# Kernel optimization log

Hardware: AMD Instinct MI355X
Metric: run time of the kernel (lower is better)

## Reference

```python
import jax, jax.numpy as jnp
import numpy as np

B, T, C, H = 2, 2048, 1024, 16
D = C // H  # head_dim = 64
CH = C // 2


def _ln(x, g, b, eps=1e-5):
    m = x.mean(-1, keepdims=True)
    v = ((x - m) ** 2).mean(-1, keepdims=True)
    return (x - m) / jnp.sqrt(v + eps) * g + b


def setup_inputs() -> dict:
    key = jax.random.key(0)
    ks = iter(jax.random.split(key, 32))
    w = lambda shp: jax.random.normal(next(ks), shp, dtype=jnp.float32) * 0.02
    inp = {
        'x': jax.random.normal(next(ks), (B, T, C), dtype=jnp.float32),
        'attention_mask': jnp.ones((B, T, T), dtype=jnp.int32),
        # importance_net: Linear(C,C/2), LN(C/2), GELU, Linear(C/2,1), Sigmoid
        'imp_w1': w((C, CH)), 'imp_b1': jnp.zeros((CH,)),
        'imp_g': jnp.ones((CH,)), 'imp_beta': jnp.zeros((CH,)),
        'imp_w2': w((CH, 1)), 'imp_b2': jnp.zeros((1,)),
        # reasoning_net: Linear(C,C), LN(C), GELU, Linear(C,C)
        'rsn_w1': w((C, C)), 'rsn_b1': jnp.zeros((C,)),
        'rsn_g': jnp.ones((C,)), 'rsn_beta': jnp.zeros((C,)),
        'rsn_w2': w((C, C)), 'rsn_b2': jnp.zeros((C,)),
        # attention projections
        'q_w': w((C, C)), 'q_b': jnp.zeros((C,)),
        'k_w': w((C, C)), 'k_b': jnp.zeros((C,)),
        'v_w': w((C, C)), 'v_b': jnp.zeros((C,)),
        'o_w': w((C, C)), 'o_b': jnp.zeros((C,)),
        # temp_net: Linear(C,C/2), LN(C/2), GELU, Linear(C/2,H)
        'tmp_w1': w((C, CH)), 'tmp_b1': jnp.zeros((CH,)),
        'tmp_g': jnp.ones((CH,)), 'tmp_beta': jnp.zeros((CH,)),
        'tmp_w2': w((CH, H)), 'tmp_b2': jnp.zeros((H,)),
        # output LayerNorm
        'norm_g': jnp.ones((C,)), 'norm_b': jnp.zeros((C,)),
    }
    return inp


def reference(x, attention_mask, imp_w1, imp_b1, imp_g, imp_beta, imp_w2, imp_b2,
              rsn_w1, rsn_b1, rsn_g, rsn_beta, rsn_w2, rsn_b2,
              q_w, q_b, k_w, k_b, v_w, v_b, o_w, o_b,
              tmp_w1, tmp_b1, tmp_g, tmp_beta, tmp_w2, tmp_b2,
              norm_g, norm_b):
    Bz, Tz, Cz = x.shape
    # importance gating: [B,T,1]
    h = jax.nn.gelu(_ln(x @ imp_w1 + imp_b1, imp_g, imp_beta), approximate=False)
    importance = jnp.maximum(jax.nn.sigmoid(h @ imp_w2 + imp_b2), 1e-6)
    xi = x * importance
    # reasoning net on gated input
    h = jax.nn.gelu(_ln(xi @ rsn_w1 + rsn_b1, rsn_g, rsn_beta), approximate=False)
    reasoned = h @ rsn_w2 + rsn_b2
    # projections
    q = (reasoned @ q_w + q_b).reshape(Bz, Tz, H, D).transpose(0, 2, 1, 3)
    k = (xi @ k_w + k_b).reshape(Bz, Tz, H, D).transpose(0, 2, 1, 3)
    v = (x @ v_w + v_b).reshape(Bz, Tz, H, D).transpose(0, 2, 1, 3)
    # per-(batch,head) temperature
    ht = jax.nn.gelu(_ln(reasoned.mean(axis=1) @ tmp_w1 + tmp_b1, tmp_g, tmp_beta), approximate=False)
    temp = jax.nn.softplus(ht @ tmp_w2 + tmp_b2) + 0.5  # [B,H]
    # attention with mask and learned temperature before softmax
    scale = 1.0 / jnp.sqrt(jnp.float32(D))
    attn = jnp.einsum('bhqd,bhkd->bhqk', q, k) * scale
    attn = jnp.where(attention_mask[:, None] == 0, -jnp.inf, attn)
    attn = attn * temp[:, :, None, None]
    attn = jax.nn.softmax(attn, axis=-1)
    # dropout is identity in eval mode
    out = jnp.einsum('bhqk,bhkd->bhqd', attn, v)
    out = out.transpose(0, 2, 1, 3).reshape(Bz, Tz, Cz)
    out = out @ o_w + o_b
    return _ln(x + out, norm_g, norm_b)
```

## Files before the change

kernel.cpp:

```cpp
#include <hip/hip_runtime.h>
#include <hip/hip_bf16.h>
#include <math.h>

#define BB 2
#define TT 2048
#define CC 1024
#define HH 16
#define DD 64
#define CHALF 512
#define NN (BB * TT)
#define LOG2E 1.44269504088896340736f

typedef __attribute__((ext_vector_type(8))) short short8;
typedef __attribute__((ext_vector_type(4))) short short4_t;
typedef __attribute__((ext_vector_type(4))) float f32x4;

__device__ __forceinline__ float gelu_exact(float x) {
    return 0.5f * x * (1.0f + erff(x * 0.70710678118654752f));
}

__device__ __forceinline__ short f2bf(float f) {
    __hip_bfloat16 h = __float2bfloat16(f);
    short s;
    __builtin_memcpy(&s, &h, 2);
    return s;
}

__device__ __forceinline__ short4_t pack_bf16x4(float a, float b, float c,
                                                float d) {
    short4_t s4;
    s4[0] = f2bf(a);
    s4[1] = f2bf(b);
    s4[2] = f2bf(c);
    s4[3] = f2bf(d);
    return s4;
}

__device__ __forceinline__ void async_copy16(const void* g, void* l) {
    __builtin_amdgcn_global_load_lds(
        (const __attribute__((address_space(1))) void*)g,
        (__attribute__((address_space(3))) void*)l, 16, 0, 0);
}

__global__ __launch_bounds__(256) void prep(
    const float* __restrict__ x, __hip_bfloat16* __restrict__ x_bf,
    const int* __restrict__ mask, int* __restrict__ flags,
    const float* w0, const float* w1, const float* w2, const float* w3,
    const float* w4, const float* w5, const float* w6,
    __hip_bfloat16* t0, __hip_bfloat16* t1, __hip_bfloat16* t2,
    __hip_bfloat16* t3, __hip_bfloat16* t4, __hip_bfloat16* t5,
    __hip_bfloat16* t6) {
    __shared__ float T[64][65];
    int blk = blockIdx.x;
    int tid = threadIdx.x;
    if (blk < 2048) {
        int i = (blk * 256 + tid) * 8;
        float4 a = *(const float4*)&x[i];
        float4 b = *(const float4*)&x[i + 4];
        __hip_bfloat16 o[8] = {
            __float2bfloat16(a.x), __float2bfloat16(a.y),
            __float2bfloat16(a.z), __float2bfloat16(a.w),
            __float2bfloat16(b.x), __float2bfloat16(b.y),
            __float2bfloat16(b.z), __float2bfloat16(b.w)};
        *(float4*)&x_bf[i] = *(float4*)o;
    } else if (blk < 4096) {
        int idx = blk - 2048;
        int kt = idx & 31, qt = (idx >> 5) & 31, b = idx >> 10;
        int* red = (int*)T;
        int r = tid >> 2;
        int c0 = (tid & 3) * 16;
        const int* base =
            mask + ((size_t)(b * TT + qt * 64 + r)) * TT + kt * 64 + c0;
        int all = 1;
#pragma unroll
        for (int i = 0; i < 4; ++i) {
            int4 m4 = *(const int4*)(base + i * 4);
            all &= (m4.x != 0) & (m4.y != 0) & (m4.z != 0) & (m4.w != 0);
        }
        red[tid] = all;
        __syncthreads();
#pragma unroll
        for (int o = 128; o > 0; o >>= 1) {
            if (tid < o) red[tid] &= red[tid + o];
            __syncthreads();
        }
        if (tid == 0) flags[(b * 32 + qt) * 32 + kt] = red[0];
    } else {
        int idx = blk - 4096;
        const float* W;
        __hip_bfloat16* Wt;
        int N, n0, k0;
        if (idx < 128) {
            W = w0; Wt = t0; N = 512;
            n0 = (idx & 7) * 64;
            k0 = (idx >> 3) * 64;
        } else {
            idx -= 128;
            int w = idx >> 8;
            int r = idx & 255;
            N = 1024;
            n0 = (r & 15) * 64;
            k0 = (r >> 4) * 64;
            switch (w) {
                case 0: W = w1; Wt = t1; break;
                case 1: W = w2; Wt = t2; break;
                case 2: W = w3; Wt = t3; break;
                case 3: W = w4; Wt = t4; break;
                case 4: W = w5; Wt = t5; break;
                default: W = w6; Wt = t6; break;
            }
        }
        int c = tid & 63, r4 = tid >> 6;
#pragma unroll
        for (int i = 0; i < 16; ++i) {
            int row = i * 4 + r4;
            T[row][c] = W[(size_t)(k0 + row) * N + n0 + c];
        }
        __syncthreads();
#pragma unroll
        for (int i = 0; i < 16; ++i) {
            int row = i * 4 + r4;
            Wt[(size_t)(n0 + row) * CC + k0 + c] = __float2bfloat16(T[c][row]);
        }
    }
}

template <bool BF16OUT>
__global__ __launch_bounds__(256) void gemm_mfma64(
    const short* __restrict__ A, const short* __restrict__ Wt,
    const float* __restrict__ bias, float* __restrict__ Cf,
    __hip_bfloat16* __restrict__ Cb, int M, int N, int K) {
    __shared__ short As0[64][32], As1[64][32];
    __shared__ short Bs0[128][32], Bs1[128][32];
    int tid = threadIdx.x;
    int wave = tid >> 6, lane = tid & 63;
    int m16 = lane & 15, quad = lane >> 4;
    int wm = wave >> 1, wn = wave & 1;
    int row0 = blockIdx.y * 64, col0 = blockIdx.x * 128;
    int lr = lane >> 2;
    int kof = (lane & 3) * 8;

    f32x4 acc[2][4];
#pragma unroll
    for (int i = 0; i < 2; ++i)
#pragma unroll
        for (int j = 0; j < 4; ++j) acc[i][j] = (f32x4){0.f, 0.f, 0.f, 0.f};

    for (int k0 = 0; k0 < K; k0 += 64) {
        const short* arow = A + (size_t)(row0 + wave * 16 + lr) * K + k0 + kof;
        async_copy16(arow, &As0[wave * 16][0]);
        async_copy16(arow + 32, &As1[wave * 16][0]);
#pragma unroll
        for (int j = 0; j < 2; ++j) {
            int rbase = wave * 32 + j * 16;
            const short* brow =
                Wt + (size_t)(col0 + rbase + lr) * K + k0 + kof;
            async_copy16(brow, &Bs0[rbase][0]);
            async_copy16(brow + 32, &Bs1[rbase][0]);
        }
        __syncthreads();
#pragma unroll
        for (int kc = 0; kc < 2; ++kc) {
            short8 af[2], bfr[4];
#pragma unroll
            for (int i = 0; i < 2; ++i)
                af[i] = kc ? *(const short8*)&As1[wm * 32 + i * 16 + m16][quad * 8]
                           : *(const short8*)&As0[wm * 32 + i * 16 + m16][quad * 8];
#pragma unroll
            for (int j = 0; j < 4; ++j)
                bfr[j] = kc ? *(const short8*)&Bs1[wn * 64 + j * 16 + m16][quad * 8]
                            : *(const short8*)&Bs0[wn * 64 + j * 16 + m16][quad * 8];
#pragma unroll
            for (int i = 0; i < 2; ++i)
#pragma unroll
                for (int j = 0; j < 4; ++j)
                    acc[i][j] = __builtin_amdgcn_mfma_f32_16x16x32_bf16(
                        af[i], bfr[j], acc[i][j], 0, 0, 0);
        }
        __syncthreads();
    }
#pragma unroll
    for (int i = 0; i < 2; ++i) {
#pragma unroll
        for (int j = 0; j < 4; ++j) {
            int col = col0 + wn * 64 + j * 16 + m16;
            float bv = bias[col];
#pragma unroll
            for (int rr = 0; rr < 4; ++rr) {
                int row = row0 + wm * 32 + i * 16 + quad * 4 + rr;
                float val = acc[i][j][rr] + bv;
                if (BF16OUT)
                    Cb[(size_t)row * N + col] = __float2bfloat16(val);
                else
                    Cf[(size_t)row * N + col] = val;
            }
        }
    }
}

__global__ __launch_bounds__(256) void gemm_qkv(
    const short* __restrict__ Aq, const short* __restrict__ Ak,
    const short* __restrict__ Av, const short* __restrict__ Wq,
    const short* __restrict__ Wk, const short* __restrict__ Wv,
    const float* __restrict__ bq, const float* __restrict__ bk,
    const float* __restrict__ bv, __hip_bfloat16* __restrict__ Cq,
    __hip_bfloat16* __restrict__ Ck, __hip_bfloat16* __restrict__ Cv,
    const float* __restrict__ tmp) {
    int z = blockIdx.z;
    const short* A = (z == 0) ? Aq : (z == 1) ? Ak : Av;
    const short* Wt = (z == 0) ? Wq : (z == 1) ? Wk : Wv;
    const float* bias = (z == 0) ? bq : (z == 1) ? bk : bv;

    __shared__ short As[128][32];
    __shared__ short Bs[128][32];
    int tid = threadIdx.x;
    int wave = tid >> 6, lane = tid & 63;
    int m16 = lane & 15, quad = lane >> 4;
    int wm = wave >> 1, wn = wave & 1;
    int row0 = blockIdx.y * 128, col0 = blockIdx.x * 128;
    int lr = lane >> 2;
    int kof = (lane & 3) * 8;

    float scale = 1.0f;
    if (z == 0)
        scale = tmp[(row0 >> 11) * HH + (col0 >> 6) + wn] * 0.125f * LOG2E;

    f32x4 acc[4][4];
#pragma unroll
    for (int i = 0; i < 4; ++i)
#pragma unroll
        for (int j = 0; j < 4; ++j) acc[i][j] = (f32x4){0.f, 0.f, 0.f, 0.f};

    for (int k0 = 0; k0 < CC; k0 += 32) {
#pragma unroll
        for (int j = 0; j < 2; ++j) {
            int rbase = wave * 32 + j * 16;
            async_copy16(A + (size_t)(row0 + rbase + lr) * CC + k0 + kof,
                         &As[rbase][0]);
            async_copy16(Wt + (size_t)(col0 + rbase + lr) * CC + k0 + kof,
                         &Bs[rbase][0]);
        }
        __syncthreads();
        short8 af[4], bfr[4];
#pragma unroll
        for (int i = 0; i < 4; ++i)
            af[i] = *(const short8*)&As[wm * 64 + i * 16 + m16][quad * 8];
#pragma unroll
        for (int j = 0; j < 4; ++j)
            bfr[j] = *(const short8*)&Bs[wn * 64 + j * 16 + m16][quad * 8];
#pragma unroll
        for (int i = 0; i < 4; ++i)
#pragma unroll
            for (int j = 0; j < 4; ++j)
                acc[i][j] = __builtin_amdgcn_mfma_f32_16x16x32_bf16(
                    af[i], bfr[j], acc[i][j], 0, 0, 0);
        __syncthreads();
    }
    if (z == 2) {
        int b = row0 >> 11;
        int t0r = (row0 & (TT - 1)) + wm * 64 + quad * 4;
#pragma unroll
        for (int i = 0; i < 4; ++i) {
#pragma unroll
            for (int j = 0; j < 4; ++j) {
                int col = col0 + wn * 64 + j * 16 + m16;
                int h = col >> 6, d = col & 63;
                float bv2 = bias[col];
                short4_t pk = pack_bf16x4(
                    acc[i][j][0] + bv2, acc[i][j][1] + bv2,
                    acc[i][j][2] + bv2, acc[i][j][3] + bv2);
                *(short4_t*)&Cv[(((size_t)(b * HH + h) * DD) + d) * TT + t0r +
                                i * 16] = pk;
            }
        }
    } else {
        __hip_bfloat16* C = (z == 0) ? Cq : Ck;
#pragma unroll
        for (int i = 0; i < 4; ++i) {
#pragma unroll
            for (int j = 0; j < 4; ++j) {
                int col = col0 + wn * 64 + j * 16 + m16;
                float bv2 = bias[col];
#pragma unroll
                for (int rr = 0; rr < 4; ++rr) {
                    int row = row0 + wm * 64 + i * 16 + quad * 4 + rr;
                    C[(size_t)row * CC + col] =
                        __float2bfloat16((acc[i][j][rr] + bv2) * scale);
                }
            }
        }
    }
}

__global__ __launch_bounds__(256) void imp_fused(
    const float* __restrict__ h1, const float* __restrict__ g,
    const float* __restrict__ beta, const float* __restrict__ w2,
    const float* __restrict__ b2, const float* __restrict__ x,
    __hip_bfloat16* __restrict__ xi) {
    int row = blockIdx.x;
    int tid = threadIdx.x;
    const float* hr = h1 + (size_t)row * CHALF;
    float v0 = hr[tid], v1 = hr[tid + 256];
    __shared__ float red[256];
    red[tid] = v0 + v1;
    __syncthreads();
#pragma unroll
    for (int o = 128; o > 0; o >>= 1) {
        if (tid < o) red[tid] += red[tid + o];
        __syncthreads();
    }
    float mean = red[0] * (1.0f / CHALF);
    __syncthreads();
    float d0 = v0 - mean, d1 = v1 - mean;
    red[tid] = d0 * d0 + d1 * d1;
    __syncthreads();
#pragma unroll
    for (int o = 128; o > 0; o >>= 1) {
        if (tid < o) red[tid] += red[tid + o];
        __syncthreads();
    }
    float inv = rsqrtf(red[0] * (1.0f / CHALF) + 1e-5f);
    __syncthreads();
    float ge0 = gelu_exact(d0 * inv * g[tid] + beta[tid]);
    float ge1 = gelu_exact(d1 * inv * g[tid + 256] + beta[tid + 256]);
    red[tid] = ge0 * w2[tid] + ge1 * w2[tid + 256];
    __syncthreads();
#pragma unroll
    for (int o = 128; o > 0; o >>= 1) {
        if (tid < o) red[tid] += red[tid + o];
        __syncthreads();
    }
    float z = red[0] + b2[0];
    float sg = 1.0f / (1.0f + expf(-z));
    float imp = fmaxf(sg, 1e-6f);
#pragma unroll
    for (int i = 0; i < 4; ++i) {
        int c = i * 256 + tid;
        xi[(size_t)row * CC + c] =
            __float2bfloat16(x[(size_t)row * CC + c] * imp);
    }
}

template <int WIDTH>
__global__ __launch_bounds__(256) void ln_gelu_bf16(
    const float* __restrict__ Y, const float* __restrict__ g,
    const float* __restrict__ beta, __hip_bfloat16* __restrict__ O) {
    constexpr int PT = WIDTH / 256;
    int row = blockIdx.x;
    int tid = threadIdx.x;
    const float* yr = Y + (size_t)row * WIDTH;
    float v[PT];
    float s = 0.f;
#pragma unroll
    for (int i = 0; i < PT; ++i) {
        v[i] = yr[i * 256 + tid];
        s += v[i];
    }
    __shared__ float red[256];
    red[tid] = s;
    __syncthreads();
#pragma unroll
    for (int o = 128; o > 0; o >>= 1) {
        if (tid < o) red[tid] += red[tid + o];
        __syncthreads();
    }
    float mean = red[0] * (1.0f / WIDTH);
    __syncthreads();
    s = 0.f;
#pragma unroll
    for (int i = 0; i < PT; ++i) {
        float d = v[i] - mean;
        s += d * d;
    }
    red[tid] = s;
    __syncthreads();
#pragma unroll
    for (int o = 128; o > 0; o >>= 1) {
        if (tid < o) red[tid] += red[tid + o];
        __syncthreads();
    }
    float inv = rsqrtf(red[0] * (1.0f / WIDTH) + 1e-5f);
#pragma unroll
    for (int i = 0; i < PT; ++i) {
        int c = i * 256 + tid;
        O[(size_t)row * WIDTH + c] =
            __float2bfloat16(gelu_exact((v[i] - mean) * inv * g[c] + beta[c]));
    }
}

__global__ __launch_bounds__(256) void mean_part(
    const __hip_bfloat16* __restrict__ R, float* __restrict__ part) {
    int idx = blockIdx.x * 256 + threadIdx.x;
    int c = idx & (CC - 1);
    int chunk = (idx >> 10) & 15;
    int b = idx >> 14;
    const __hip_bfloat16* base = R + ((size_t)(b * TT + chunk * 128)) * CC + c;
    float s = 0.f;
    for (int t = 0; t < 128; ++t) s += __bfloat162float(base[(size_t)t * CC]);
    part[idx] = s;
}

__global__ __launch_bounds__(256) void temp_gemv1(
    const float* __restrict__ part, const float* __restrict__ w1,
    const float* __restrict__ b1, float* __restrict__ acc1) {
    __shared__ float rm_l[CC];
    __shared__ float red[256];
    int b = blockIdx.y;
    int c0 = blockIdx.x * 64;
    int tid = threadIdx.x;
    for (int cc = tid; cc < CC; cc += 256) {
        float s = 0.f;
#pragma unroll
        for (int ch = 0; ch < 16; ++ch)
            s += part[(size_t)(b * 16 + ch) * CC + cc];
        rm_l[cc] = s * (1.0f / TT);
    }
    __syncthreads();
    int col = c0 + (tid & 63);
    int kq = tid >> 6;
    float s = 0.f;
#pragma unroll 8
    for (int i = kq * 256; i < kq * 256 + 256; ++i)
        s = fmaf(rm_l[i], w1[(size_t)i * CHALF + col], s);
    red[tid] = s;
    __syncthreads();
    if (tid < 64) {
        float t = red[tid] + red[tid + 64] + red[tid + 128] + red[tid + 192];
        acc1[b * CHALF + tid + c0] = t + b1[col];
    }
}

__global__ __launch_bounds__(512) void temp_fin(
    const float* __restrict__ acc1, const float* __restrict__ g,
    const float* __restrict__ beta, const float* __restrict__ w2,
    const float* __restrict__ b2, float* __restrict__ temp) {
    __shared__ float red[512];
    __shared__ float wred[8][16];
    int b = blockIdx.x;
    int tid = threadIdx.x;
    int wave = tid >> 6, lane = tid & 63;
    float acc = acc1[b * CHALF + tid];
    red[tid] = acc;
    __syncthreads();
#pragma unroll
    for (int o = 256; o > 0; o >>= 1) {
        if (tid < o) red[tid] += red[tid + o];
        __syncthreads();
    }
    float mean = red[0] * (1.0f / CHALF);
    __syncthreads();
    float d = acc - mean;
    red[tid] = d * d;
    __syncthreads();
#pragma unroll
    for (int o = 256; o > 0; o >>= 1) {
        if (tid < o) red[tid] += red[tid + o];
        __syncthreads();
    }
    float inv = rsqrtf(red[0] * (1.0f / CHALF) + 1e-5f);
    float ht = gelu_exact((acc - mean) * inv * g[tid] + beta[tid]);
    float p[16];
#pragma unroll
    for (int j = 0; j < 16; ++j) p[j] = ht * w2[tid * HH + j];
#pragma unroll
    for (int off = 1; off < 64; off <<= 1)
#pragma unroll
        for (int j = 0; j < 16; ++j) p[j] += __shfl_xor(p[j], off, 64);
    if (lane == 0)
#pragma unroll
        for (int j = 0; j < 16; ++j) wred[wave][j] = p[j];
    __syncthreads();
    if (tid < HH) {
        float s = b2[tid];
#pragma unroll
        for (int w = 0; w < 8; ++w) s += wred[w][tid];
        float sp = fmaxf(s, 0.f) + log1pf(expf(-fabsf(s)));
        temp[b * HH + tid] = sp + 0.5f;
    }
}

__global__ __launch_bounds__(256) void flash_attn_mfma(
    const short* __restrict__ q, const short* __restrict__ k,
    const short* __restrict__ vt, const int* __restrict__ mask,
    const int* __restrict__ flags, __hip_bfloat16* __restrict__ out) {
    __shared__ short Ks[64][72];
    __shared__ short Vt[64][72];
    __shared__ short Ps[128][72];
    int tid = threadIdx.x;
    int wave = tid >> 6, lane = tid & 63;
    int m16 = lane & 15, quad = lane >> 4;
    int qt = blockIdx.x;
    int q0 = qt * 128;
    int bh = blockIdx.y;
    int b = bh >> 4, h = bh & 15;

    short8 qf[2][2];
#pragma unroll
    for (int qg = 0; qg < 2; ++qg) {
        const short* qrow = q + ((size_t)(b * TT + q0 + wave * 32 + qg * 16 + m16)) * CC +
                            h * DD + quad * 8;
        qf[qg][0] = *(const short8*)(qrow);
        qf[qg][1] = *(const short8*)(qrow + 32);
    }

    float m_run[2] = {-INFINITY, -INFINITY};
    float l_run[2] = {0.f, 0.f};
    f32x4 acc_o[2][4];
#pragma unroll
    for (int qg = 0; qg < 2; ++qg)
#pragma unroll
        for (int t = 0; t < 4; ++t) acc_o[qg][t] = (f32x4){0.f, 0.f, 0.f, 0.f};

    for (int kt = 0; kt < TT / 64; ++kt) {
        int kb = kt * 64;
#pragma unroll
        for (int i = 0; i < 2; ++i) {
            int idx = i * 256 + tid;
            int r = idx >> 3;
            int dc = (idx & 7) * 8;
            *(short8*)&Ks[r][dc] =
                *(const short8*)(k + ((size_t)(b * TT + kb + r)) * CC + h * DD + dc);
            *(short8*)&Vt[r][dc] =
                *(const short8*)(vt + ((size_t)bh * DD + r) * TT + kb + dc);
        }
        __syncthreads();

        short8 kf[4][2];
#pragma unroll
        for (int t = 0; t < 4; ++t) {
            kf[t][0] = *(const short8*)&Ks[t * 16 + m16][quad * 8];
            kf[t][1] = *(const short8*)&Ks[t * 16 + m16][32 + quad * 8];
        }
        int fl = flags[(b * 32 + 2 * qt + (wave >> 1)) * 32 + kt];

#pragma unroll
        for (int qg = 0; qg < 2; ++qg) {
            f32x4 sacc[4];
#pragma unroll
            for (int t = 0; t < 4; ++t) sacc[t] = (f32x4){0.f, 0.f, 0.f, 0.f};
#pragma unroll
            for (int t = 0; t < 4; ++t) {
                sacc[t] = __builtin_amdgcn_mfma_f32_16x16x32_bf16(kf[t][0], qf[qg][0], sacc[t], 0, 0, 0);
                sacc[t] = __builtin_amdgcn_mfma_f32_16x16x32_bf16(kf[t][1], qf[qg][1], sacc[t], 0, 0, 0);
            }
            float sv[4][4];
#pragma unroll
            for (int t = 0; t < 4; ++t)
#pragma unroll
                for (int r = 0; r < 4; ++r) sv[t][r] = sacc[t][r];
            if (fl == 0) {
                int qrow = q0 + wave * 32 + qg * 16 + m16;
#pragma unroll
                for (int t = 0; t < 4; ++t)
#pragma unroll
                    for (int r = 0; r < 4; ++r) {
                        int kg = kb + t * 16 + quad * 4 + r;
                        if (mask[((size_t)(b * TT + qrow)) * TT + kg] == 0)
                            sv[t][r] = -INFINITY;
                    }
            }
            float mx = sv[0][0];
#pragma unroll
            for (int t = 0; t < 4; ++t)
#pragma unroll
                for (int r = 0; r < 4; ++r) mx = fmaxf(mx, sv[t][r]);
            mx = fmaxf(mx, __shfl_xor(mx, 16, 64));
            mx = fmaxf(mx, __shfl_xor(mx, 32, 64));
            float mnew = fmaxf(m_run[qg], mx);
            if (__any(mnew > m_run[qg])) {
                float alpha = __builtin_amdgcn_exp2f(m_run[qg] - mnew);
                l_run[qg] *= alpha;
#pragma unroll
                for (int td = 0; td < 4; ++td)
#pragma unroll
                    for (int r = 0; r < 4; ++r) acc_o[qg][td][r] *= alpha;
            }
            m_run[qg] = mnew;
            int prow = wave * 32 + qg * 16 + m16;
            float psum = 0.f;
#pragma unroll
            for (int t = 0; t < 4; ++t) {
                short4_t pk;
#pragma unroll
                for (int r = 0; r < 4; ++r) {
                    float p = __builtin_amdgcn_exp2f(sv[t][r] - mnew);
                    psum += p;
                    pk[r] = f2bf(p);
                }
                *(short4_t*)&Ps[prow][t * 16 + quad * 4] = pk;
            }
            psum += __shfl_xor(psum, 16, 64);
            psum += __shfl_xor(psum, 32, 64);
            l_run[qg] += psum;
        }

#pragma unroll
        for (int kc = 0; kc < 2; ++kc) {
            short8 vf[4];
#pragma unroll
            for (int td = 0; td < 4; ++td)
                vf[td] = *(const short8*)&Vt[td * 16 + m16][kc * 32 + quad * 8];
#pragma unroll
            for (int qg = 0; qg < 2; ++qg) {
                short8 pf = *(const short8*)&Ps[wave * 32 + qg * 16 + m16][kc * 32 + quad * 8];
#pragma unroll
                for (int td = 0; td < 4; ++td)
                    acc_o[qg][td] = __builtin_amdgcn_mfma_f32_16x16x32_bf16(
                        vf[td], pf, acc_o[qg][td], 0, 0, 0);
            }
        }
        __syncthreads();
    }

#pragma unroll
    for (int qg = 0; qg < 2; ++qg) {
        float inv = 1.0f / l_run[qg];
        int row = b * TT + q0 + wave * 32 + qg * 16 + m16;
#pragma unroll
        for (int td = 0; td < 4; ++td) {
            short4_t pk = pack_bf16x4(
                acc_o[qg][td][0] * inv, acc_o[qg][td][1] * inv,
                acc_o[qg][td][2] * inv, acc_o[qg][td][3] * inv);
            *(short4_t*)&out[(size_t)row * CC + h * DD + td * 16 + quad * 4] = pk;
        }
    }
}

__global__ __launch_bounds__(256) void final_ln(
    const float* __restrict__ x, const float* __restrict__ p,
    const float* __restrict__ g, const float* __restrict__ beta,
    float* __restrict__ out) {
    int row = blockIdx.x;
    int tid = threadIdx.x;
    const float* xr = x + (size_t)row * CC;
    const float* pr = p + (size_t)row * CC;
    float v[4];
    float s = 0.f;
#pragma unroll
    for (int i = 0; i < 4; ++i) {
        int c = i * 256 + tid;
        v[i] = xr[c] + pr[c];
        s += v[i];
    }
    __shared__ float red[256];
    red[tid] = s;
    __syncthreads();
#pragma unroll
    for (int o = 128; o > 0; o >>= 1) {
        if (tid < o) red[tid] += red[tid + o];
        __syncthreads();
    }
    float mean = red[0] * (1.0f / CC);
    __syncthreads();
    s = 0.f;
#pragma unroll
    for (int i = 0; i < 4; ++i) {
        float d = v[i] - mean;
        s += d * d;
    }
    red[tid] = s;
    __syncthreads();
#pragma unroll
    for (int o = 128; o > 0; o >>= 1) {
        if (tid < o) red[tid] += red[tid + o];
        __syncthreads();
    }
    float inv = rsqrtf(red[0] * (1.0f / CC) + 1e-5f);
#pragma unroll
    for (int i = 0; i < 4; ++i) {
        int c = i * 256 + tid;
        out[(size_t)row * CC + c] = (v[i] - mean) * inv * g[c] + beta[c];
    }
}

extern "C" void kernel_launch(void* const* d_in, const int* in_sizes, int n_in,
                              void* d_out, int out_size, void* d_ws,
                              size_t ws_size, hipStream_t stream) {
    const float* x        = (const float*)d_in[0];
    const int*   mask     = (const int*)d_in[1];
    const float* imp_w1   = (const float*)d_in[2];
    const float* imp_b1   = (const float*)d_in[3];
    const float* imp_g    = (const float*)d_in[4];
    const float* imp_beta = (const float*)d_in[5];
    const float* imp_w2   = (const float*)d_in[6];
    const float* imp_b2   = (const float*)d_in[7];
    const float* rsn_w1   = (const float*)d_in[8];
    const float* rsn_b1   = (const float*)d_in[9];
    const float* rsn_g    = (const float*)d_in[10];
    const float* rsn_beta = (const float*)d_in[11];
    const float* rsn_w2   = (const float*)d_in[12];
    const float* rsn_b2   = (const float*)d_in[13];
    const float* q_w      = (const float*)d_in[14];
    const float* q_b      = (const float*)d_in[15];
    const float* k_w      = (const float*)d_in[16];
    const float* k_b      = (const float*)d_in[17];
    const float* v_w      = (const float*)d_in[18];
    const float* v_b      = (const float*)d_in[19];
    const float* o_w      = (const float*)d_in[20];
    const float* o_b      = (const float*)d_in[21];
    const float* tmp_w1   = (const float*)d_in[22];
    const float* tmp_b1   = (const float*)d_in[23];
    const float* tmp_g    = (const float*)d_in[24];
    const float* tmp_beta = (const float*)d_in[25];
    const float* tmp_w2   = (const float*)d_in[26];
    const float* tmp_b2   = (const float*)d_in[27];
    const float* norm_g   = (const float*)d_in[28];
    const float* norm_b   = (const float*)d_in[29];
    float* out = (float*)d_out;
    float* ws  = (float*)d_ws;

    float* h1  = ws;
    float* h2  = ws + 2097152;
    __hip_bfloat16* x_bf  = (__hip_bfloat16*)(ws + 6291456);
    __hip_bfloat16* xi_bf = (__hip_bfloat16*)(ws + 8388608);
    __hip_bfloat16* h2b   = (__hip_bfloat16*)(ws + 10485760);
    __hip_bfloat16* rs_bf = (__hip_bfloat16*)(ws + 12582912);
    __hip_bfloat16* qb    = (__hip_bfloat16*)(ws + 14680064);
    __hip_bfloat16* kb    = (__hip_bfloat16*)(ws + 16777216);
    __hip_bfloat16* vtb   = (__hip_bfloat16*)(ws + 20971520);
    __hip_bfloat16* imp_w1t = (__hip_bfloat16*)(ws + 23068672);
    __hip_bfloat16* rsn_w1t = (__hip_bfloat16*)(ws + 23330816);
    __hip_bfloat16* rsn_w2t = (__hip_bfloat16*)(ws + 23855104);
    __hip_bfloat16* q_wt    = (__hip_bfloat16*)(ws + 24379392);
    __hip_bfloat16* k_wt    = (__hip_bfloat16*)(ws + 24903680);
    __hip_bfloat16* v_wt    = (__hip_bfloat16*)(ws + 25427968);
    __hip_bfloat16* o_wt    = (__hip_bfloat16*)(ws + 25952256);
    float* tmp  = ws + 26478592;
    float* part = ws + 26479104;
    int*   flg  = (int*)(ws + 26511872);
    float* acc1 = ws + 26513920;

    dim3 blk(256);
    prep<<<5760, blk, 0, stream>>>(
        x, x_bf, mask, flg,
        imp_w1, rsn_w1, rsn_w2, q_w, k_w, v_w, o_w,
        imp_w1t, rsn_w1t, rsn_w2t, q_wt, k_wt, v_wt, o_wt);

    gemm_mfma64<false><<<dim3(CHALF / 128, NN / 64), blk, 0, stream>>>(
        (const short*)x_bf, (const short*)imp_w1t, imp_b1, h1, nullptr, NN, CHALF, CC);
    imp_fused<<<NN, blk, 0, stream>>>(h1, imp_g, imp_beta, imp_w2, imp_b2, x, xi_bf);
    gemm_mfma64<false><<<dim3(CC / 128, NN / 64), blk, 0, stream>>>(
        (const short*)xi_bf, (const short*)rsn_w1t, rsn_b1, h2, nullptr, NN, CC, CC);
    ln_gelu_bf16<CC><<<NN, blk, 0, stream>>>(h2, rsn_g, rsn_beta, h2b);
    gemm_mfma64<true><<<dim3(CC / 128, NN / 64), blk, 0, stream>>>(
        (const short*)h2b, (const short*)rsn_w2t, rsn_b2, nullptr, rs_bf, NN, CC, CC);
    mean_part<<<128, blk, 0, stream>>>(rs_bf, part);
    temp_gemv1<<<dim3(CHALF / 64, BB), blk, 0, stream>>>(part, tmp_w1, tmp_b1, acc1);
    temp_fin<<<BB, dim3(512), 0, stream>>>(acc1, tmp_g, tmp_beta, tmp_w2, tmp_b2, tmp);
    gemm_qkv<<<dim3(CC / 128, NN / 128, 3), blk, 0, stream>>>(
        (const short*)rs_bf, (const short*)xi_bf, (const short*)x_bf,
        (const short*)q_wt, (const short*)k_wt, (const short*)v_wt,
        q_b, k_b, v_b, qb, kb, vtb, tmp);
    flash_attn_mfma<<<dim3(TT / 128, BB * HH), blk, 0, stream>>>(
        (const short*)qb, (const short*)kb, (const short*)vtb, mask, flg, rs_bf);
    gemm_mfma64<false><<<dim3(CC / 128, NN / 64), blk, 0, stream>>>(
        (const short*)rs_bf, (const short*)o_wt, o_b, h2, nullptr, NN, CC, CC);
    final_ln<<<NN, blk, 0, stream>>>(x, h2, norm_g, norm_b, out);
}
```

Baseline: 413.9 us.

## Store GEMM intermediates as bf16, vectorize LN kernels, double K-step in QKV GEMM

Two GEMM outputs that feed LayerNorm (the reasoning-net first layer and the output projection) now write bf16 instead of fp32. The following LN kernels read bf16 with vectorized 4-wide loads and stores. The QKV GEMM loads 64 K-columns per iteration into two LDS buffers, halving the number of barrier pairs. Together these cut intermediate memory traffic and sync overhead, at the cost of extra bf16 rounding before the residual add and the LayerNorm statistics.

```diff
diff --git a/kernel.cpp b/kernel.cpp
--- a/kernel.cpp
+++ b/kernel.cpp
@@ -24,6 +24,12 @@
     short s;
     __builtin_memcpy(&s, &h, 2);
     return s;
+}
+
+__device__ __forceinline__ float bf2f(short s) {
+    __hip_bfloat16 h;
+    __builtin_memcpy(&h, &s, 2);
+    return __bfloat162float(h);
 }
 
 __device__ __forceinline__ short4_t pack_bf16x4(float a, float b, float c,
@@ -211,8 +217,8 @@
     const short* Wt = (z == 0) ? Wq : (z == 1) ? Wk : Wv;
     const float* bias = (z == 0) ? bq : (z == 1) ? bk : bv;
 
-    __shared__ short As[128][32];
-    __shared__ short Bs[128][32];
+    __shared__ short As0[128][32], As1[128][32];
+    __shared__ short Bs0[128][32], Bs1[128][32];
     int tid = threadIdx.x;
     int wave = tid >> 6, lane = tid & 63;
     int m16 = lane & 15, quad = lane >> 4;
@@ -231,29 +237,36 @@
 #pragma unroll
         for (int j = 0; j < 4; ++j) acc[i][j] = (f32x4){0.f, 0.f, 0.f, 0.f};
 
-    for (int k0 = 0; k0 < CC; k0 += 32) {
+    for (int k0 = 0; k0 < CC; k0 += 64) {
 #pragma unroll
         for (int j = 0; j < 2; ++j) {
             int rbase = wave * 32 + j * 16;
-            async_copy16(A + (size_t)(row0 + rbase + lr) * CC + k0 + kof,
-                         &As[rbase][0]);
-            async_copy16(Wt + (size_t)(col0 + rbase + lr) * CC + k0 + kof,
-                         &Bs[rbase][0]);
-        }
-        __syncthreads();
-        short8 af[4], bfr[4];
-#pragma unroll
-        for (int i = 0; i < 4; ++i)
-            af[i] = *(const short8*)&As[wm * 64 + i * 16 + m16][quad * 8];
-#pragma unroll
-        for (int j = 0; j < 4; ++j)
-            bfr[j] = *(const short8*)&Bs[wn * 64 + j * 16 + m16][quad * 8];
-#pragma unroll
-        for (int i = 0; i < 4; ++i)
+            const short* ar = A + (size_t)(row0 + rbase + lr) * CC + k0 + kof;
+            async_copy16(ar, &As0[rbase][0]);
+            async_copy16(ar + 32, &As1[rbase][0]);
+            const short* br = Wt + (size_t)(col0 + rbase + lr) * CC + k0 + kof;
+            async_copy16(br, &Bs0[rbase][0]);
+            async_copy16(br + 32, &Bs1[rbase][0]);
+        }
+        __syncthreads();
+#pragma unroll
+        for (int kc = 0; kc < 2; ++kc) {
+            short8 af[4], bfr[4];
+#pragma unroll
+            for (int i = 0; i < 4; ++i)
+                af[i] = kc ? *(const short8*)&As1[wm * 64 + i * 16 + m16][quad * 8]
+                           : *(const short8*)&As0[wm * 64 + i * 16 + m16][quad * 8];
 #pragma unroll
             for (int j = 0; j < 4; ++j)
-                acc[i][j] = __builtin_amdgcn_mfma_f32_16x16x32_bf16(
-                    af[i], bfr[j], acc[i][j], 0, 0, 0);
+                bfr[j] = kc ? *(const short8*)&Bs1[wn * 64 + j * 16 + m16][quad * 8]
+                            : *(const short8*)&Bs0[wn * 64 + j * 16 + m16][quad * 8];
+#pragma unroll
+            for (int i = 0; i < 4; ++i)
+#pragma unroll
+                for (int j = 0; j < 4; ++j)
+                    acc[i][j] = __builtin_amdgcn_mfma_f32_16x16x32_bf16(
+                        af[i], bfr[j], acc[i][j], 0, 0, 0);
+        }
         __syncthreads();
     }
     if (z == 2) {
@@ -341,19 +354,18 @@
     }
 }
 
-template <int WIDTH>
-__global__ __launch_bounds__(256) void ln_gelu_bf16(
-    const float* __restrict__ Y, const float* __restrict__ g,
+__global__ __launch_bounds__(256) void ln_gelu_bb(
+    const __hip_bfloat16* __restrict__ Y, const float* __restrict__ g,
     const float* __restrict__ beta, __hip_bfloat16* __restrict__ O) {
-    constexpr int PT = WIDTH / 256;
     int row = blockIdx.x;
     int tid = threadIdx.x;
-    const float* yr = Y + (size_t)row * WIDTH;
-    float v[PT];
+    int c0 = tid * 4;
+    short4_t raw = *(const short4_t*)&Y[(size_t)row * CC + c0];
+    float v[4];
     float s = 0.f;
 #pragma unroll
-    for (int i = 0; i < PT; ++i) {
-        v[i] = yr[i * 256 + tid];
+    for (int i = 0; i < 4; ++i) {
+        v[i] = bf2f(raw[i]);
         s += v[i];
     }
     __shared__ float red[256];
@@ -364,11 +376,11 @@
         if (tid < o) red[tid] += red[tid + o];
         __syncthreads();
     }
-    float mean = red[0] * (1.0f / WIDTH);
+    float mean = red[0] * (1.0f / CC);
     __syncthreads();
     s = 0.f;
 #pragma unroll
-    for (int i = 0; i < PT; ++i) {
+    for (int i = 0; i < 4; ++i) {
         float d = v[i] - mean;
         s += d * d;
     }
@@ -379,13 +391,15 @@
         if (tid < o) red[tid] += red[tid + o];
         __syncthreads();
     }
-    float inv = rsqrtf(red[0] * (1.0f / WIDTH) + 1e-5f);
-#pragma unroll
-    for (int i = 0; i < PT; ++i) {
-        int c = i * 256 + tid;
-        O[(size_t)row * WIDTH + c] =
-            __float2bfloat16(gelu_exact((v[i] - mean) * inv * g[c] + beta[c]));
-    }
+    float inv = rsqrtf(red[0] * (1.0f / CC) + 1e-5f);
+    float4 gg = *(const float4*)&g[c0];
+    float4 bb = *(const float4*)&beta[c0];
+    short4_t ov = pack_bf16x4(
+        gelu_exact((v[0] - mean) * inv * gg.x + bb.x),
+        gelu_exact((v[1] - mean) * inv * gg.y + bb.y),
+        gelu_exact((v[2] - mean) * inv * gg.z + bb.z),
+        gelu_exact((v[3] - mean) * inv * gg.w + bb.w));
+    *(short4_t*)&O[(size_t)row * CC + c0] = ov;
 }
 
 __global__ __launch_bounds__(256) void mean_part(
@@ -626,22 +640,18 @@
     }
 }
 
-__global__ __launch_bounds__(256) void final_ln(
-    const float* __restrict__ x, const float* __restrict__ p,
+__global__ __launch_bounds__(256) void final_ln_b(
+    const float* __restrict__ x, const __hip_bfloat16* __restrict__ p,
     const float* __restrict__ g, const float* __restrict__ beta,
     float* __restrict__ out) {
     int row = blockIdx.x;
     int tid = threadIdx.x;
-    const float* xr = x + (size_t)row * CC;
-    const float* pr = p + (size_t)row * CC;
-    float v[4];
-    float s = 0.f;
-#pragma unroll
-    for (int i = 0; i < 4; ++i) {
-        int c = i * 256 + tid;
-        v[i] = xr[c] + pr[c];
-        s += v[i];
-    }
+    int c0 = tid * 4;
+    float4 xv = *(const float4*)&x[(size_t)row * CC + c0];
+    short4_t pv = *(const short4_t*)&p[(size_t)row * CC + c0];
+    float v[4] = {xv.x + bf2f(pv[0]), xv.y + bf2f(pv[1]),
+                  xv.z + bf2f(pv[2]), xv.w + bf2f(pv[3])};
+    float s = v[0] + v[1] + v[2] + v[3];
     __shared__ float red[256];
     red[tid] = s;
     __syncthreads();
@@ -666,11 +676,13 @@
         __syncthreads();
     }
     float inv = rsqrtf(red[0] * (1.0f / CC) + 1e-5f);
-#pragma unroll
-    for (int i = 0; i < 4; ++i) {
-        int c = i * 256 + tid;
-        out[(size_t)row * CC + c] = (v[i] - mean) * inv * g[c] + beta[c];
-    }
+    float4 gg = *(const float4*)&g[c0];
+    float4 bb = *(const float4*)&beta[c0];
+    float4 ov = {(v[0] - mean) * inv * gg.x + bb.x,
+                 (v[1] - mean) * inv * gg.y + bb.y,
+                 (v[2] - mean) * inv * gg.z + bb.z,
+                 (v[3] - mean) * inv * gg.w + bb.w};
+    *(float4*)&out[(size_t)row * CC + c0] = ov;
 }
 
 extern "C" void kernel_launch(void* const* d_in, const int* in_sizes, int n_in,
@@ -710,7 +722,7 @@
     float* ws  = (float*)d_ws;
 
     float* h1  = ws;
-    float* h2  = ws + 2097152;
+    __hip_bfloat16* g1b   = (__hip_bfloat16*)(ws + 2097152);
     __hip_bfloat16* x_bf  = (__hip_bfloat16*)(ws + 6291456);
     __hip_bfloat16* xi_bf = (__hip_bfloat16*)(ws + 8388608);
     __hip_bfloat16* h2b   = (__hip_bfloat16*)(ws + 10485760);
@@ -739,9 +751,9 @@
     gemm_mfma64<false><<<dim3(CHALF / 128, NN / 64), blk, 0, stream>>>(
         (const short*)x_bf, (const short*)imp_w1t, imp_b1, h1, nullptr, NN, CHALF, CC);
     imp_fused<<<NN, blk, 0, stream>>>(h1, imp_g, imp_beta, imp_w2, imp_b2, x, xi_bf);
-    gemm_mfma64<false><<<dim3(CC / 128, NN / 64), blk, 0, stream>>>(
-        (const short*)xi_bf, (const short*)rsn_w1t, rsn_b1, h2, nullptr, NN, CC, CC);
-    ln_gelu_bf16<CC><<<NN, blk, 0, stream>>>(h2, rsn_g, rsn_beta, h2b);
+    gemm_mfma64<true><<<dim3(CC / 128, NN / 64), blk, 0, stream>>>(
+        (const short*)xi_bf, (const short*)rsn_w1t, rsn_b1, nullptr, g1b, NN, CC, CC);
+    ln_gelu_bb<<<NN, blk, 0, stream>>>(g1b, rsn_g, rsn_beta, h2b);
     gemm_mfma64<true><<<dim3(CC / 128, NN / 64), blk, 0, stream>>>(
         (const short*)h2b, (const short*)rsn_w2t, rsn_b2, nullptr, rs_bf, NN, CC, CC);
     mean_part<<<128, blk, 0, stream>>>(rs_bf, part);
@@ -753,7 +765,7 @@
         q_b, k_b, v_b, qb, kb, vtb, tmp);
     flash_attn_mfma<<<dim3(TT / 128, BB * HH), blk, 0, stream>>>(
         (const short*)qb, (const short*)kb, (const short*)vtb, mask, flg, rs_bf);
-    gemm_mfma64<false><<<dim3(CC / 128, NN / 64), blk, 0, stream>>>(
-        (const short*)rs_bf, (const short*)o_wt, o_b, h2, nullptr, NN, CC, CC);
-    final_ln<<<NN, blk, 0, stream>>>(x, h2, norm_g, norm_b, out);
-}
+    gemm_mfma64<true><<<dim3(CC / 128, NN / 64), blk, 0, stream>>>(
+        (const short*)rs_bf, (const short*)o_wt, o_b, nullptr, g1b, NN, CC, CC);
+    final_ln_b<<<NN, blk, 0, stream>>>(x, g1b, norm_g, norm_b, out);
+}
```

Result: no change. 412.7 us (median of 2 runs) (-0.3%).
